# Kernel optimization log

Measured on AMD Instinct MI355X. Metric: run time of the kernel, lower is better.

## Reference

```python
import jax, jax.numpy as jnp
import numpy as np

B, T, N, K = 8, 1024, 64, 8


def _normalize_logprob(logmat, axis):
    # temperature = 1 in forward_backward
    norm = jax.scipy.special.logsumexp(logmat, axis=axis, keepdims=True)
    return logmat - norm, norm


def setup_inputs() -> dict:
    key = jax.random.key(0)
    k1, k2, k3 = jax.random.split(key, 3)
    log_a = jax.random.normal(k1, (B, T, N, K, K), dtype=jnp.float32)
    log_b = jax.random.normal(k2, (B, T, N, K), dtype=jnp.float32)
    logprob_z1 = jax.random.normal(k3, (N, K), dtype=jnp.float32)
    return {"log_a": log_a, "log_b": log_b, "logprob_z1": logprob_z1}


def reference(log_a, log_b, logprob_z1):
    # log_a: (B,T,N,K,K)  transition log-probs a[t][i,j] = p(z_t=i | z_{t-1}=j)
    # log_b: (B,T,N,K)    emission log-likelihoods
    # logprob_z1: (N,K)   initial state log-prob (Z_init parameter)
    b_tm = jnp.moveaxis(log_b, 1, 0)  # (T,B,N,K) time-major for scan
    a_tm = jnp.moveaxis(log_a, 1, 0)  # (T,B,N,K,K)

    # ---- forward recursion ----
    alpha0, norm0 = _normalize_logprob(logprob_z1[None] + log_b[:, 0], -1)  # (B,N,K),(B,N,1)

    def fstep(prev, xs):
        b_t, a_t = xs  # (B,N,K), (B,N,K,K)
        # alpha_t[i] = logsumexp_j( b_t[i] + a_t[i,j] + prev[j] )
        u = jax.scipy.special.logsumexp(
            b_t[..., :, None] + a_t + prev[..., None, :], axis=-1)
        alpha, nrm = _normalize_logprob(u, -1)
        return alpha, (alpha, nrm)

    _, (alphas, fnorms) = jax.lax.scan(fstep, alpha0, (b_tm[1:], a_tm[1:]))
    forward_probs = jnp.moveaxis(
        jnp.concatenate([alpha0[None], alphas], axis=0), 0, 1)  # (B,T,N,K)

    # ---- backward recursion ----
    betaT = jnp.zeros_like(alpha0)  # (B,N,K)

    def bstep(nxt, xs):
        b_tp1, a_tp1 = xs  # (B,N,K), (B,N,K,K)
        # beta_t[j] = logsumexp_i( nxt[i] + a_tp1[i,j] + b_tp1[i] )
        u = jax.scipy.special.logsumexp(
            nxt[..., :, None] + a_tp1 + b_tp1[..., :, None], axis=-2)
        beta, nrm = _normalize_logprob(u, -1)
        return beta, (beta, nrm)

    _, (betas, bnorms) = jax.lax.scan(
        bstep, betaT, (b_tm[1:], a_tm[1:]), reverse=True)
    backward_probs = jnp.moveaxis(
        jnp.concatenate([betas, betaT[None]], axis=0), 0, 1)  # (B,T,N,K)

    # ---- posteriors ----
    gamma1, _ = _normalize_logprob(forward_probs + backward_probs, -1)  # (B,T,N,K)

    # gamma2[t][i,j] ~ beta_t[i] + a_t[i,j] + b_t[i] + alpha_{t-1}[j], t >= 1
    g2u = (forward_probs[:, :-1, :, None, :]      # (B,T-1,N,1,K)
           + backward_probs[:, 1:, :, :, None]    # (B,T-1,N,K,1)
           + log_a[:, 1:]                         # (B,T-1,N,K,K)
           + log_b[:, 1:][..., None])             # (B,T-1,N,K,1)
    g2_norm = jax.scipy.special.logsumexp(g2u, axis=(-2, -1), keepdims=True)
    gamma2_unpad = g2u - g2_norm
    gamma2 = jnp.concatenate(
        [jnp.zeros_like(gamma2_unpad[:, :1]), gamma2_unpad], axis=1)  # (B,T,N,K,K)

    return forward_probs, backward_probs, gamma1, gamma2
```

## Files before the change

### kernel.cpp

```cpp
#include <hip/hip_runtime.h>

#define Tdim 1024
#define Ndim 64
#define FSZ (8 * 1024 * 64 * 8)

typedef unsigned uint2v __attribute__((ext_vector_type(2)));

#define DPPADD(v, ctrl) ((v) + __int_as_float(__builtin_amdgcn_update_dpp( \
    0, __float_as_int(v), ctrl, 0xF, 0xF, false)))

__device__ __forceinline__ float swap_add16(float v) {
  unsigned u = __float_as_uint(v);
  uint2v r = __builtin_amdgcn_permlane16_swap(u, u, false, false);
  return __uint_as_float(r[0]) + __uint_as_float(r[1]);
}
__device__ __forceinline__ float swap_add32(float v) {
  unsigned u = __float_as_uint(v);
  uint2v r = __builtin_amdgcn_permlane32_swap(u, u, false, false);
  return __uint_as_float(r[0]) + __uint_as_float(r[1]);
}

#define SUM_LO3(v) { v = DPPADD(v, 0xB1); v = DPPADD(v, 0x4E); v = DPPADD(v, 0x141); }
#define SUM_HI3(v) { v = DPPADD(v, 0x128); v = swap_add16(v); v = swap_add32(v); }

#define GLOAD_LDS(gp, lp) __builtin_amdgcn_global_load_lds( \
    (const __attribute__((address_space(1))) unsigned*)(gp), \
    (__attribute__((address_space(3))) unsigned*)(lp), 4, 0, 0)


__device__ __forceinline__ void stage_fwd(const float* __restrict__ a_base,
                                          const float* __restrict__ b_base,
                                          int t0, int swz, int lane,
                                          float* sA, float* sB) {
  asm volatile("s_waitcnt lgkmcnt(0)" ::: "memory");
#pragma unroll
  for (int s = 0; s < 16; ++s) {
    int t = t0 + s; if (t > Tdim - 1) t = Tdim - 1;
    GLOAD_LDS(&a_base[(size_t)t * (Ndim * 64) + swz], &sA[s * 64]);
  }
#pragma unroll
  for (int h = 0; h < 2; ++h) {
    int tb = t0 + h * 8 + (lane >> 3); if (tb > Tdim - 1) tb = Tdim - 1;
    GLOAD_LDS(&b_base[(size_t)tb * (Ndim * 8) + (lane & 7)], &sB[h * 64]);
  }
}

__device__ __forceinline__ void stage_bwd(const float* __restrict__ a_base,
                                          const float* __restrict__ b_base,
                                          int t0, int swz, int lane,
                                          float* sA, float* sB) {
  asm volatile("s_waitcnt lgkmcnt(0)" ::: "memory");
#pragma unroll
  for (int s = 0; s < 16; ++s) {
    int t = t0 - s; if (t < 0) t = 0;
    GLOAD_LDS(&a_base[(size_t)t * (Ndim * 64) + swz], &sA[s * 64]);
  }
#pragma unroll
  for (int h = 0; h < 2; ++h) {
    int tb = t0 - 1 - (h * 8 + (lane >> 3)); if (tb < 0) tb = 0;
    GLOAD_LDS(&b_base[(size_t)tb * (Ndim * 8) + (lane & 7)], &sB[h * 64]);
  }
}

__device__ __forceinline__ void fwd_compute_lds(int t0, int x, int y, int swz, int trw,
                                                const float* sA, const float* sB,
                                                float& q, float& sc,
                                                float* __restrict__ f_base) {
  float av[4], bv[4];
#pragma unroll
  for (int p = 0; p < 4; ++p) {
    av[p] = sA[p * 64 + ((p & 1) ? trw : swz)];
    bv[p] = sB[p * 8 + ((p & 1) ? y : x)];
  }
#pragma unroll
  for (int s = 0; s < 16; ++s) {
    int t = t0 + s;
    float a = av[s & 3], bb = bv[s & 3];
    if (s + 4 < 16) {
      int p = s + 4;
      av[s & 3] = sA[p * 64 + ((p & 1) ? trw : swz)];
      bv[s & 3] = sB[p * 8 + ((p & 1) ? y : x)];
    }
    if (t < Tdim) {
      int oidx = (s & 1) ? y : x;
      float v = __expf(a) * q;
      if (!(s & 1)) { SUM_LO3(v); } else { SUM_HI3(v); }
      float S = v * (__expf(bb) * sc);
      q = S;
      float T = S;
      if (!(s & 1)) { SUM_HI3(T); } else { SUM_LO3(T); }
      sc = __builtin_amdgcn_rcpf(T);
      float la = __logf(S * sc);
      if ((((s & 1) ? x : y)) == 0) f_base[(size_t)t * (Ndim * 8) + oidx] = la;
    }
  }
}

__device__ __forceinline__ void bwd_compute_lds(int t0, int x, int y, int swz, int trw,
                                                const float* sA, const float* sB,
                                                float& u, float& sc,
                                                float* __restrict__ bo) {
  float av[4], bv[4];
#pragma unroll
  for (int p = 0; p < 4; ++p) {
    av[p] = sA[p * 64 + ((p & 1) ? trw : swz)];
    bv[p] = sB[p * 8 + ((p & 1) ? x : y)];
  }
#pragma unroll
  for (int s = 0; s < 16; ++s) {
    int tau = t0 - s;
    float a = av[s & 3], bb = bv[s & 3];
    if (s + 4 < 16) {
      int p = s + 4;
      av[s & 3] = sA[p * 64 + ((p & 1) ? trw : swz)];
      bv[s & 3] = sB[p * 8 + ((p & 1) ? x : y)];
    }
    if (tau >= 1) {
      float v = __expf(a) * u;
      if (!(s & 1)) { SUM_HI3(v); } else { SUM_LO3(v); }
      int oidx = (s & 1) ? x : y;
      float unew = (__expf(bb) * sc) * v;
      float W = v;
      if (!(s & 1)) { SUM_LO3(W); } else { SUM_HI3(W); }
      float scn = __builtin_amdgcn_rcpf(W);
      float lb = __logf(v * scn);
      if ((((s & 1) ? y : x)) == 0) bo[(size_t)(tau - 1) * (Ndim * 8) + oidx] = lb;
      u = unew;
      sc = scn;
    }
  }
}

__global__ __launch_bounds__(64, 1) void chains_kernel(const float* __restrict__ A,
                                                       const float* __restrict__ Bm,
                                                       const float* __restrict__ Z1,
                                                       float* __restrict__ Fout,
                                                       float* __restrict__ Bout) {
  __shared__ float sA0[1024], sA1[1024], sB0[128], sB1[128];
  const int lane = threadIdx.x;
  const int x = lane >> 3, y = lane & 7;
  const int swz = (x << 3) | (y ^ x);
  const int trw = (y << 3) | (x ^ y);
  const int chain = blockIdx.x & 511;
  const int b = chain >> 6, n = chain & 63;
  const size_t cbase = ((size_t)b * Tdim) * Ndim + n;
  const float* a_base = A + cbase * 64;
  const float* b_base = Bm + cbase * 8;

  if (blockIdx.x < 512) {
    float* f_base = Fout + cbase * 8;
    float v0 = Z1[n * 8 + y] + b_base[y];
    float q = __expf(v0);
    float T0 = q; SUM_LO3(T0);
    if (x == 0) f_base[y] = v0 - __logf(T0);
    float sc = __builtin_amdgcn_rcpf(T0);
    stage_fwd(a_base, b_base, 1, swz, lane, sA0, sB0);
#pragma unroll 1
    for (int kk = 0; kk < 64; kk += 2) {
      stage_fwd(a_base, b_base, 1 + (kk + 1) * 16, swz, lane, sA1, sB1);
      fwd_compute_lds(1 + kk * 16, x, y, swz, trw, sA0, sB0, q, sc, f_base);
      if (kk + 2 < 64) stage_fwd(a_base, b_base, 1 + (kk + 2) * 16, swz, lane, sA0, sB0);
      fwd_compute_lds(1 + (kk + 1) * 16, x, y, swz, trw, sA1, sB1, q, sc, f_base);
    }
  } else {
    float* bo = Bout + cbase * 8;
    float bT = b_base[(size_t)(Tdim - 1) * (Ndim * 8) + x];
    float u = __expf(bT);
    if (x == 0) bo[(size_t)(Tdim - 1) * (Ndim * 8) + y] = 0.f;
    float sc = 1.0f;
    stage_bwd(a_base, b_base, Tdim - 1, swz, lane, sA0, sB0);
#pragma unroll 1
    for (int kk = 0; kk < 64; kk += 2) {
      stage_bwd(a_base, b_base, Tdim - 1 - (kk + 1) * 16, swz, lane, sA1, sB1);
      bwd_compute_lds(Tdim - 1 - kk * 16, x, y, swz, trw, sA0, sB0, u, sc, bo);
      if (kk + 2 < 64) stage_bwd(a_base, b_base, Tdim - 1 - (kk + 2) * 16, swz, lane, sA0, sB0);
      bwd_compute_lds(Tdim - 1 - (kk + 1) * 16, x, y, swz, trw, sA1, sB1, u, sc, bo);
    }
  }
}

__global__ __launch_bounds__(256) void gamma_kernel(const float* __restrict__ A,
                                                    const float* __restrict__ Bm,
                                                    const float* __restrict__ F,
                                                    const float* __restrict__ Bo,
                                                    float* __restrict__ G1,
                                                    float* __restrict__ G2) {
  const int lane = threadIdx.x & 63;
  const int i = lane & 7;
  const int gq = lane >> 3;
  const int g = (blockIdx.x * 4 + (threadIdx.x >> 6)) * 8 + gq;
  const int t = (g >> 6) & (Tdim - 1);

  const float bo_i = Bo[(size_t)g * 8 + i];

  {
    float u1 = F[(size_t)g * 8 + i] + bo_i;
    float s1 = __expf(u1);
    SUM_LO3(s1);
    G1[(size_t)g * 8 + i] = u1 - __logf(s1);
  }

  float4* o = (float4*)&G2[(size_t)g * 64 + i * 8];
  if (t == 0) {
    float4 z = make_float4(0.f, 0.f, 0.f, 0.f);
    o[0] = z; o[1] = z;
  } else {
    const float4* ap = (const float4*)&A[(size_t)g * 64 + i * 8];
    float4 a0 = ap[0], a1 = ap[1];
    const float4* fp = (const float4*)&F[((size_t)g - Ndim) * 8];
    float4 f0 = fp[0], f1 = fp[1];
    float c = bo_i + Bm[(size_t)g * 8 + i];
    float v0 = c + a0.x + f0.x, v1 = c + a0.y + f0.y;
    float v2 = c + a0.z + f0.z, v3 = c + a0.w + f0.w;
    float v4 = c + a1.x + f1.x, v5 = c + a1.y + f1.y;
    float v6 = c + a1.z + f1.z, v7 = c + a1.w + f1.w;
    float r = ((__expf(v0) + __expf(v1)) + (__expf(v2) + __expf(v3)))
            + ((__expf(v4) + __expf(v5)) + (__expf(v6) + __expf(v7)));
    SUM_LO3(r);
    float lq = __logf(r);
    o[0] = make_float4(v0 - lq, v1 - lq, v2 - lq, v3 - lq);
    o[1] = make_float4(v4 - lq, v5 - lq, v6 - lq, v7 - lq);
  }
}

extern "C" void kernel_launch(void* const* d_in, const int* in_sizes, int n_in,
                              void* d_out, int out_size, void* d_ws, size_t ws_size,
                              hipStream_t stream) {
  const float* A  = (const float*)d_in[0];
  const float* Bm = (const float*)d_in[1];
  const float* Z1 = (const float*)d_in[2];
  float* out = (float*)d_out;
  float* Fout = out;
  float* Bout = out + FSZ;
  float* G1   = out + 2 * FSZ;
  float* G2   = out + 3 * FSZ;

  chains_kernel<<<dim3(1024), dim3(64), 0, stream>>>(A, Bm, Z1, Fout, Bout);
  gamma_kernel<<<dim3(8 * Tdim * Ndim / 32), dim3(256), 0, stream>>>(A, Bm, Fout, Bout, G1, G2);
}
```

Measured before the change: 451.8 us.

## Batch LDS reads per 16-step tile and stage chain outputs through LDS

The forward and backward chain loops are restructured. Each 16-step tile now reads all of its A/B values from LDS into registers first, then issues the next tile's global-to-LDS prefetch, using sched_barriers to fix that order. The per-step scattered global stores of the log outputs are replaced by writes into a small LDS buffer, which is flushed with two coalesced stores per tile. The explicit lgkmcnt waits in the staging helpers are dropped, which relies on the compiler inserting the correct waits and risks a race between LDS writes and reads without explicit synchronisation.

```diff
diff --git a/kernel.cpp b/kernel.cpp
--- a/kernel.cpp
+++ b/kernel.cpp
@@ -32,7 +32,6 @@
                                           const float* __restrict__ b_base,
                                           int t0, int swz, int lane,
                                           float* sA, float* sB) {
-  asm volatile("s_waitcnt lgkmcnt(0)" ::: "memory");
 #pragma unroll
   for (int s = 0; s < 16; ++s) {
     int t = t0 + s; if (t > Tdim - 1) t = Tdim - 1;
@@ -49,7 +48,6 @@
                                           const float* __restrict__ b_base,
                                           int t0, int swz, int lane,
                                           float* sA, float* sB) {
-  asm volatile("s_waitcnt lgkmcnt(0)" ::: "memory");
 #pragma unroll
   for (int s = 0; s < 16; ++s) {
     int t = t0 - s; if (t < 0) t = 0;
@@ -59,75 +57,6 @@
   for (int h = 0; h < 2; ++h) {
     int tb = t0 - 1 - (h * 8 + (lane >> 3)); if (tb < 0) tb = 0;
     GLOAD_LDS(&b_base[(size_t)tb * (Ndim * 8) + (lane & 7)], &sB[h * 64]);
-  }
-}
-
-__device__ __forceinline__ void fwd_compute_lds(int t0, int x, int y, int swz, int trw,
-                                                const float* sA, const float* sB,
-                                                float& q, float& sc,
-                                                float* __restrict__ f_base) {
-  float av[4], bv[4];
-#pragma unroll
-  for (int p = 0; p < 4; ++p) {
-    av[p] = sA[p * 64 + ((p & 1) ? trw : swz)];
-    bv[p] = sB[p * 8 + ((p & 1) ? y : x)];
-  }
-#pragma unroll
-  for (int s = 0; s < 16; ++s) {
-    int t = t0 + s;
-    float a = av[s & 3], bb = bv[s & 3];
-    if (s + 4 < 16) {
-      int p = s + 4;
-      av[s & 3] = sA[p * 64 + ((p & 1) ? trw : swz)];
-      bv[s & 3] = sB[p * 8 + ((p & 1) ? y : x)];
-    }
-    if (t < Tdim) {
-      int oidx = (s & 1) ? y : x;
-      float v = __expf(a) * q;
-      if (!(s & 1)) { SUM_LO3(v); } else { SUM_HI3(v); }
-      float S = v * (__expf(bb) * sc);
-      q = S;
-      float T = S;
-      if (!(s & 1)) { SUM_HI3(T); } else { SUM_LO3(T); }
-      sc = __builtin_amdgcn_rcpf(T);
-      float la = __logf(S * sc);
-      if ((((s & 1) ? x : y)) == 0) f_base[(size_t)t * (Ndim * 8) + oidx] = la;
-    }
-  }
-}
-
-__device__ __forceinline__ void bwd_compute_lds(int t0, int x, int y, int swz, int trw,
-                                                const float* sA, const float* sB,
-                                                float& u, float& sc,
-                                                float* __restrict__ bo) {
-  float av[4], bv[4];
-#pragma unroll
-  for (int p = 0; p < 4; ++p) {
-    av[p] = sA[p * 64 + ((p & 1) ? trw : swz)];
-    bv[p] = sB[p * 8 + ((p & 1) ? x : y)];
-  }
-#pragma unroll
-  for (int s = 0; s < 16; ++s) {
-    int tau = t0 - s;
-    float a = av[s & 3], bb = bv[s & 3];
-    if (s + 4 < 16) {
-      int p = s + 4;
-      av[s & 3] = sA[p * 64 + ((p & 1) ? trw : swz)];
-      bv[s & 3] = sB[p * 8 + ((p & 1) ? x : y)];
-    }
-    if (tau >= 1) {
-      float v = __expf(a) * u;
-      if (!(s & 1)) { SUM_HI3(v); } else { SUM_LO3(v); }
-      int oidx = (s & 1) ? x : y;
-      float unew = (__expf(bb) * sc) * v;
-      float W = v;
-      if (!(s & 1)) { SUM_LO3(W); } else { SUM_HI3(W); }
-      float scn = __builtin_amdgcn_rcpf(W);
-      float lb = __logf(v * scn);
-      if ((((s & 1) ? y : x)) == 0) bo[(size_t)(tau - 1) * (Ndim * 8) + oidx] = lb;
-      u = unew;
-      sc = scn;
-    }
   }
 }
 
@@ -136,7 +65,7 @@
                                                        const float* __restrict__ Z1,
                                                        float* __restrict__ Fout,
                                                        float* __restrict__ Bout) {
-  __shared__ float sA0[1024], sA1[1024], sB0[128], sB1[128];
+  __shared__ float sA0[1024], sA1[1024], sB0[128], sB1[128], sLa[128];
   const int lane = threadIdx.x;
   const int x = lane >> 3, y = lane & 7;
   const int swz = (x << 3) | (y ^ x);
@@ -156,11 +85,40 @@
     float sc = __builtin_amdgcn_rcpf(T0);
     stage_fwd(a_base, b_base, 1, swz, lane, sA0, sB0);
 #pragma unroll 1
-    for (int kk = 0; kk < 64; kk += 2) {
-      stage_fwd(a_base, b_base, 1 + (kk + 1) * 16, swz, lane, sA1, sB1);
-      fwd_compute_lds(1 + kk * 16, x, y, swz, trw, sA0, sB0, q, sc, f_base);
-      if (kk + 2 < 64) stage_fwd(a_base, b_base, 1 + (kk + 2) * 16, swz, lane, sA0, sB0);
-      fwd_compute_lds(1 + (kk + 1) * 16, x, y, swz, trw, sA1, sB1, q, sc, f_base);
+    for (int kk = 0; kk < 64; ++kk) {
+      const float* sA = (kk & 1) ? sA1 : sA0;
+      const float* sB = (kk & 1) ? sB1 : sB0;
+      float* nA = (kk & 1) ? sA0 : sA1;
+      float* nB = (kk & 1) ? sB0 : sB1;
+      const int t0 = 1 + kk * 16;
+      float av[16], bv[16];
+#pragma unroll
+      for (int s = 0; s < 16; ++s) {
+        av[s] = sA[s * 64 + ((s & 1) ? trw : swz)];
+        bv[s] = sB[s * 8 + ((s & 1) ? y : x)];
+      }
+      __builtin_amdgcn_sched_barrier(0);
+      if (kk + 1 < 64) stage_fwd(a_base, b_base, t0 + 16, swz, lane, nA, nB);
+      __builtin_amdgcn_sched_barrier(0);
+#pragma unroll
+      for (int s = 0; s < 16; ++s) {
+        int oidx = (s & 1) ? y : x;
+        float v = __expf(av[s]) * q;
+        if (!(s & 1)) { SUM_LO3(v); } else { SUM_HI3(v); }
+        float S = v * (__expf(bv[s]) * sc);
+        q = S;
+        float T = S;
+        if (!(s & 1)) { SUM_HI3(T); } else { SUM_LO3(T); }
+        sc = __builtin_amdgcn_rcpf(T);
+        float la = __logf(S * sc);
+        if ((((s & 1) ? x : y)) == 0) sLa[s * 8 + oidx] = la;
+      }
+      __builtin_amdgcn_sched_barrier(0);
+#pragma unroll
+      for (int h = 0; h < 2; ++h) {
+        int t = t0 + x + h * 8;
+        if (t < Tdim) f_base[(size_t)t * (Ndim * 8) + y] = sLa[h * 64 + lane];
+      }
     }
   } else {
     float* bo = Bout + cbase * 8;
@@ -170,11 +128,41 @@
     float sc = 1.0f;
     stage_bwd(a_base, b_base, Tdim - 1, swz, lane, sA0, sB0);
 #pragma unroll 1
-    for (int kk = 0; kk < 64; kk += 2) {
-      stage_bwd(a_base, b_base, Tdim - 1 - (kk + 1) * 16, swz, lane, sA1, sB1);
-      bwd_compute_lds(Tdim - 1 - kk * 16, x, y, swz, trw, sA0, sB0, u, sc, bo);
-      if (kk + 2 < 64) stage_bwd(a_base, b_base, Tdim - 1 - (kk + 2) * 16, swz, lane, sA0, sB0);
-      bwd_compute_lds(Tdim - 1 - (kk + 1) * 16, x, y, swz, trw, sA1, sB1, u, sc, bo);
+    for (int kk = 0; kk < 64; ++kk) {
+      const float* sA = (kk & 1) ? sA1 : sA0;
+      const float* sB = (kk & 1) ? sB1 : sB0;
+      float* nA = (kk & 1) ? sA0 : sA1;
+      float* nB = (kk & 1) ? sB0 : sB1;
+      const int t0 = Tdim - 1 - kk * 16;
+      float av[16], bv[16];
+#pragma unroll
+      for (int s = 0; s < 16; ++s) {
+        av[s] = sA[s * 64 + ((s & 1) ? trw : swz)];
+        bv[s] = sB[s * 8 + ((s & 1) ? x : y)];
+      }
+      __builtin_amdgcn_sched_barrier(0);
+      if (kk + 1 < 64) stage_bwd(a_base, b_base, t0 - 16, swz, lane, nA, nB);
+      __builtin_amdgcn_sched_barrier(0);
+#pragma unroll
+      for (int s = 0; s < 16; ++s) {
+        float v = __expf(av[s]) * u;
+        if (!(s & 1)) { SUM_HI3(v); } else { SUM_LO3(v); }
+        int oidx = (s & 1) ? x : y;
+        float unew = (__expf(bv[s]) * sc) * v;
+        float W = v;
+        if (!(s & 1)) { SUM_LO3(W); } else { SUM_HI3(W); }
+        float scn = __builtin_amdgcn_rcpf(W);
+        float lb = __logf(v * scn);
+        if ((((s & 1) ? y : x)) == 0) sLa[s * 8 + oidx] = lb;
+        u = unew;
+        sc = scn;
+      }
+      __builtin_amdgcn_sched_barrier(0);
+#pragma unroll
+      for (int h = 0; h < 2; ++h) {
+        int trow = t0 - (x + h * 8) - 1;
+        if (trow >= 0) bo[(size_t)trow * (Ndim * 8) + y] = sLa[h * 64 + lane];
+      }
     }
   }
 }
```

After: 459.6 us. Within noise of the previous version (+1.7%).
